# Kernel optimization log

Measured on AMD Instinct MI355X. Metric: run time of the kernel, lower is better.

## Reference

```python
import jax, jax.numpy as jnp
import numpy as np

B, C, H, W = 8, 256, 64, 64
RED = 16

def setup_inputs() -> dict:
    key = jax.random.key(0)
    ks = jax.random.split(key, 10)
    s = 0.05
    return {
        "x": jax.random.normal(ks[0], (B, C, H, W), jnp.float32),
        "ca_w1": jax.random.normal(ks[1], (C // RED, C), jnp.float32) * s,
        "ca_w2": jax.random.normal(ks[2], (C, C // RED), jnp.float32) * s,
        "q_w": jax.random.normal(ks[3], (C // RED, C), jnp.float32) * s,
        "q_b": jax.random.normal(ks[4], (C // RED,), jnp.float32) * s,
        "k_w": jax.random.normal(ks[5], (C // RED, C), jnp.float32) * s,
        "k_b": jax.random.normal(ks[6], (C // RED,), jnp.float32) * s,
        "v_w": jax.random.normal(ks[7], (C, C), jnp.float32) * s,
        "v_b": jax.random.normal(ks[8], (C,), jnp.float32) * s,
        "gamma": jax.random.normal(ks[9], (1,), jnp.float32) * s,
    }

def _cbam(x, ca_w1, ca_w2, q_w, q_b, k_w, k_b, v_w, v_b, gamma):
    # ---- Channel attention (squeeze-excite with avg+max pooling) ----
    avg = jnp.mean(x, axis=(2, 3))          # [B, C]
    mx = jnp.max(x, axis=(2, 3))            # [B, C]
    def fc(s):
        h = jax.nn.relu(jnp.einsum('rc,bc->br', ca_w1, s))
        return jnp.einsum('cr,br->bc', ca_w2, h)
    gate = jax.nn.sigmoid(fc(avg) + fc(mx))[:, :, None, None]
    x = x * gate
    # ---- Spatial (non-local) attention ----
    b, c, h, w = x.shape
    hw = h * w
    xf = x.reshape(b, c, hw)                          # [B, C, HW]
    q = jnp.einsum('rc,bcn->brn', q_w, xf) + q_b[None, :, None]   # [B, C/r, HW]
    k = jnp.einsum('rc,bcn->brn', k_w, xf) + k_b[None, :, None]
    v = jnp.einsum('oc,bcn->bon', v_w, xf) + v_b[None, :, None]   # [B, C, HW]
    attn = jax.nn.softmax(jnp.einsum('bri,brj->bij', q, k), axis=-1)  # [B, HW, HW]
    out = jnp.einsum('bcj,bij->bci', v, attn).reshape(b, c, h, w)
    return gamma[0] * out + x

def reference(x, ca_w1, ca_w2, q_w, q_b, k_w, k_b, v_w, v_b, gamma):
    return _cbam(x, ca_w1, ca_w2, q_w, q_b, k_w, k_b, v_w, v_b, gamma)
```

## Files before the change

kernel.cpp:

```cpp
#include <hip/hip_runtime.h>
#include <hip/hip_bf16.h>
#include <math.h>

#define BB 8
#define CCH 256
#define HWN 4096
#define RR 16

typedef __attribute__((ext_vector_type(8))) short short8;
typedef __attribute__((ext_vector_type(4))) float f32x4;

static __device__ __forceinline__ unsigned short f2bf(float x) {
    union { float f; unsigned u; } v; v.f = x;
    return (unsigned short)((v.u + 0x8000u) >> 16);
}

__global__ __launch_bounds__(256) void k_pool(const float* __restrict__ x,
                                              float* __restrict__ avgp,
                                              float* __restrict__ maxp,
                                              const float* __restrict__ vw,
                                              const float* __restrict__ qw,
                                              const float* __restrict__ kw,
                                              unsigned short* __restrict__ Wb) {
    int bc = blockIdx.x;
    int t = threadIdx.x;
    if (bc < 288) {
        int idx = bc * 256 + t;
        int m = idx >> 8, c = idx & 255;
        float v;
        if (m < 256) v = vw[idx];
        else if (m < 272) v = qw[(m - 256) * 256 + c];
        else v = kw[(m - 272) * 256 + c];
        Wb[idx] = f2bf(v);
    }
    const float4* p = (const float4*)(x + (size_t)bc * HWN);
    float s = 0.f, m = -INFINITY;
#pragma unroll
    for (int i = 0; i < 4; ++i) {
        float4 v = p[t + 256 * i];
        s += v.x + v.y + v.z + v.w;
        m = fmaxf(m, fmaxf(fmaxf(v.x, v.y), fmaxf(v.z, v.w)));
    }
    for (int off = 32; off; off >>= 1) {
        s += __shfl_down(s, off);
        m = fmaxf(m, __shfl_down(m, off));
    }
    __shared__ float ss[4], sm[4];
    int wid = t >> 6;
    if ((t & 63) == 0) { ss[wid] = s; sm[wid] = m; }
    __syncthreads();
    if (t == 0) {
        float S = ss[0] + ss[1] + ss[2] + ss[3];
        float M = fmaxf(fmaxf(sm[0], sm[1]), fmaxf(sm[2], sm[3]));
        avgp[bc] = S * (1.f / (float)HWN);
        maxp[bc] = M;
    }
}

__global__ __launch_bounds__(256) void k_gate(const float* __restrict__ avgp,
                                              const float* __restrict__ maxp,
                                              const float* __restrict__ w1,
                                              const float* __restrict__ w2,
                                              float* __restrict__ gate) {
    int b = blockIdx.x, t = threadIdx.x;
    __shared__ float sa[CCH], sx[CCH], sh[32];
    sa[t] = avgp[b * CCH + t];
    sx[t] = maxp[b * CCH + t];
    __syncthreads();
    if (t < 32) {
        int r = t & 15;
        const float* src = (t < 16) ? sa : sx;
        float h = 0.f;
        for (int c = 0; c < CCH; ++c) h += w1[r * CCH + c] * src[c];
        sh[t] = fmaxf(h, 0.f);
    }
    __syncthreads();
    float g = 0.f;
#pragma unroll
    for (int r = 0; r < RR; ++r) g += w2[t * RR + r] * (sh[r] + sh[16 + r]);
    gate[b * CCH + t] = 1.f / (1.f + __expf(-g));
}

__global__ __launch_bounds__(256) void k_proj(const float* __restrict__ x,
                                              const float* __restrict__ gate,
                                              const unsigned short* __restrict__ Wb,
                                              const float* __restrict__ vb,
                                              const float* __restrict__ qb,
                                              const float* __restrict__ kb,
                                              unsigned short* __restrict__ qT,
                                              unsigned short* __restrict__ kT,
                                              unsigned short* __restrict__ vB) {
    int b = blockIdx.x & 7;
    int n0 = (blockIdx.x >> 3) << 6;
    int t = threadIdx.x;
    int w = t >> 6, l = t & 63, quad = l >> 4, ln = l & 15;

    __shared__ __align__(16) unsigned short xs_t[64][72];
    __shared__ __align__(16) unsigned short vtile[256 * 72];
    __shared__ float qk_s[32][66];

    const f32x4 zf = {0.f, 0.f, 0.f, 0.f};
    f32x4 acc[18];
#pragma unroll
    for (int mt = 0; mt < 18; ++mt) acc[mt] = zf;

    for (int cc = 0; cc < 4; ++cc) {
        __syncthreads();
#pragma unroll
        for (int it = 0; it < 4; ++it) {
            int idx = it * 256 + t;
            int cl = idx >> 4, nq = idx & 15;
            int c = cc * 64 + cl;
            float g = gate[b * CCH + c];
            float4 v = *(const float4*)(x + (((size_t)(b * CCH + c)) << 12) + n0 + nq * 4);
            xs_t[nq * 4 + 0][cl] = f2bf(v.x * g);
            xs_t[nq * 4 + 1][cl] = f2bf(v.y * g);
            xs_t[nq * 4 + 2][cl] = f2bf(v.z * g);
            xs_t[nq * 4 + 3][cl] = f2bf(v.w * g);
        }
        __syncthreads();

        short8 bfrag[2];
#pragma unroll
        for (int kc = 0; kc < 2; ++kc)
            bfrag[kc] = *(const short8*)&xs_t[w * 16 + ln][kc * 32 + quad * 8];

#pragma unroll
        for (int mt = 0; mt < 18; ++mt) {
#pragma unroll
            for (int kc = 0; kc < 2; ++kc) {
                short8 af = *(const short8*)(Wb + ((size_t)(mt * 16 + ln)) * 256 + cc * 64 + kc * 32 + quad * 8);
                acc[mt] = __builtin_amdgcn_mfma_f32_16x16x32_bf16(af, bfrag[kc], acc[mt], 0, 0, 0);
            }
        }
    }

#pragma unroll
    for (int mt = 0; mt < 16; ++mt) {
#pragma unroll
        for (int r = 0; r < 4; ++r) {
            int m = mt * 16 + quad * 4 + r;
            vtile[m * 72 + w * 16 + ln] = f2bf(acc[mt][r] + vb[m]);
        }
    }
#pragma unroll
    for (int r = 0; r < 4; ++r) {
        qk_s[quad * 4 + r][w * 16 + ln] = acc[16][r];
        qk_s[16 + quad * 4 + r][w * 16 + ln] = acc[17][r];
    }
    __syncthreads();

    {
        unsigned short* vBp = vB + (((size_t)b) << 20);
        int c = t;
#pragma unroll
        for (int Q = 0; Q < 8; ++Q) {
            short8 v8 = *(const short8*)(vtile + c * 72 + Q * 8);
            *(short8*)(vBp + ((size_t)((((n0 >> 3) + Q) << 8) + c) << 3)) = v8;
        }
    }
    if (t < 128) {
        int isK = t >> 6;
        int n = t & 63;
        const float* bias = isK ? kb : qb;
        unsigned u32[8];
#pragma unroll
        for (int j = 0; j < 8; ++j) {
            unsigned lo = f2bf(qk_s[isK * 16 + 2 * j][n] + bias[2 * j]);
            unsigned hi = f2bf(qk_s[isK * 16 + 2 * j + 1][n] + bias[2 * j + 1]);
            u32[j] = lo | (hi << 16);
        }
        unsigned short* dst = (isK ? kT : qT) + ((size_t)(b * HWN + n0 + n)) * RR;
        uint4 d0 = {u32[0], u32[1], u32[2], u32[3]};
        uint4 d1 = {u32[4], u32[5], u32[6], u32[7]};
        ((uint4*)dst)[0] = d0;
        ((uint4*)dst)[1] = d1;
    }
}

__global__ __launch_bounds__(512, 4) void k_attn(const unsigned short* __restrict__ qT,
                                                 const unsigned short* __restrict__ kT,
                                                 const unsigned short* __restrict__ vB,
                                                 const float* __restrict__ x,
                                                 const float* __restrict__ gate,
                                                 const float* __restrict__ gamma,
                                                 float* __restrict__ out) {
    int b = blockIdx.x & 7;
    int i0 = (blockIdx.x >> 3) << 6;
    int t = threadIdx.x;
    int w = __builtin_amdgcn_readfirstlane(t >> 6);
    int l = t & 63;
    int quad = l >> 4, ln = l & 15;
    int jsub = w >> 1;
    int ih = w & 1;
    int c0 = w * 32;

    __shared__ __align__(16) unsigned short p_lds[4][4096];
    __shared__ float l_s[4][68];

    const short8 zs = {0, 0, 0, 0, 0, 0, 0, 0};
    const f32x4 zf = {0.f, 0.f, 0.f, 0.f};

    short8 bq[2];
    bq[0] = zs; bq[1] = zs;
    if (quad < 2) {
#pragma unroll
        for (int u = 0; u < 2; ++u)
            bq[u] = *(const short8*)(qT + (((size_t)(b * HWN + i0 + ih * 32 + u * 16 + ln)) << 4) + (quad << 3));
    }

    f32x4 acc[2][4];
#pragma unroll
    for (int cs = 0; cs < 2; ++cs)
#pragma unroll
        for (int is = 0; is < 4; ++is) acc[cs][is] = zf;
    float lsum[2] = {0.f, 0.f};

    const float c1 = 1.44269504f;
    const float c0e = -11.5415603f;

    const unsigned short* kb_u = kT + ((size_t)(b * HWN)) * RR;
    const int kln = ((jsub * 16 + ln) << 4) + (quad << 3);
    const unsigned short* vb_u = vB + (((size_t)b) << 20) + ((size_t)c0 << 3);
    int vln[4];
#pragma unroll
    for (int ks = 0; ks < 2; ++ks)
#pragma unroll
        for (int cs = 0; cs < 2; ++cs)
            vln[ks * 2 + cs] = (((ks * 4 + quad) << 8) + cs * 16 + ln) << 3;

    int soff = ((jsub * 2 + (quad >> 1)) * 64 + ih * 32 + ln) * 8 + (quad & 1) * 4;
    int rbase = quad * 512 + ln * 8;

    short8 akA = zs, akB = zs;
    short8 avA[4], avB[4];

    auto load_ak = [&](short8& ak, int j0) {
        if (quad < 2) ak = *(const short8*)(kb_u + ((j0 << 4) + kln));
    };
    auto load_av = [&](short8 (&av)[4], int j0) {
        const unsigned short* vp = vb_u + (j0 << 8);
#pragma unroll
        for (int u = 0; u < 4; ++u) av[u] = *(const short8*)(vp + vln[u]);
    };

    load_ak(akA, 0);
    load_ak(akB, 64);
    load_av(avA, 0);
    load_av(avB, 64);

    auto finish_s = [&](const f32x4& sf, unsigned short* pbuf, int u) {
        float p0 = exp2f(fmaf(sf[0], c1, c0e));
        float p1 = exp2f(fmaf(sf[1], c1, c0e));
        float p2 = exp2f(fmaf(sf[2], c1, c0e));
        float p3 = exp2f(fmaf(sf[3], c1, c0e));
        lsum[u] += (p0 + p1) + (p2 + p3);
        uint2 pk;
        asm("v_cvt_pk_bf16_f32 %0, %1, %2" : "=v"(pk.x) : "v"(p0), "v"(p1));
        asm("v_cvt_pk_bf16_f32 %0, %1, %2" : "=v"(pk.y) : "v"(p2), "v"(p3));
        *(uint2*)(pbuf + soff + u * 128) = pk;
    };

    auto pv = [&](const short8 (&av)[4], const unsigned short* pbuf) {
#pragma unroll
        for (int ks = 0; ks < 2; ++ks) {
            short8 bp[4];
#pragma unroll
            for (int is = 0; is < 4; ++is)
                bp[is] = *(const short8*)(pbuf + rbase + ks * 2048 + is * 128);
#pragma unroll
            for (int cs = 0; cs < 2; ++cs)
#pragma unroll
                for (int is = 0; is < 4; ++is)
                    acc[cs][is] = __builtin_amdgcn_mfma_f32_16x16x32_bf16(av[ks * 2 + cs], bp[is], acc[cs][is], 0, 0, 0);
        }
    };

    for (int jt = 0; jt < 32; ++jt) {
        unsigned short* pb0 = &p_lds[(jt & 1) * 2 + 0][0];
        unsigned short* pb1 = &p_lds[(jt & 1) * 2 + 1][0];

        f32x4 sf00 = __builtin_amdgcn_mfma_f32_16x16x32_bf16(akA, bq[0], zf, 0, 0, 0);
        f32x4 sf01 = __builtin_amdgcn_mfma_f32_16x16x32_bf16(akA, bq[1], zf, 0, 0, 0);
        f32x4 sf10 = __builtin_amdgcn_mfma_f32_16x16x32_bf16(akB, bq[0], zf, 0, 0, 0);
        f32x4 sf11 = __builtin_amdgcn_mfma_f32_16x16x32_bf16(akB, bq[1], zf, 0, 0, 0);
        finish_s(sf00, pb0, 0);
        finish_s(sf01, pb0, 1);
        finish_s(sf10, pb1, 0);
        finish_s(sf11, pb1, 1);

        __syncthreads();

        bool pf = jt < 31;
        int j0n = (jt + 1) << 7;
        if (pf) { load_ak(akA, j0n); load_ak(akB, j0n + 64); }

        pv(avA, pb0);
        if (pf) load_av(avA, j0n);
        pv(avB, pb1);
        if (pf) load_av(avB, j0n + 64);
    }

    lsum[0] += __shfl_xor(lsum[0], 16, 64);
    lsum[0] += __shfl_xor(lsum[0], 32, 64);
    lsum[1] += __shfl_xor(lsum[1], 16, 64);
    lsum[1] += __shfl_xor(lsum[1], 32, 64);
    if (l < 16) {
        l_s[jsub][ih * 32 + l] = lsum[0];
        l_s[jsub][ih * 32 + 16 + l] = lsum[1];
    }
    __syncthreads();

    float g = gamma[0];
    float rinv[4];
#pragma unroll
    for (int is = 0; is < 4; ++is) {
        int i = is * 16 + ln;
        float lf = (l_s[0][i] + l_s[1][i]) + (l_s[2][i] + l_s[3][i]);
        rinv[is] = g / lf;
    }

#pragma unroll
    for (int cs = 0; cs < 2; ++cs) {
#pragma unroll
        for (int r = 0; r < 4; ++r) {
            int c = c0 + cs * 16 + quad * 4 + r;
            float gc = gate[b * CCH + c];
            size_t rowoff = (((size_t)(b * CCH + c)) << 12) + i0;
            float* po = out + rowoff;
            const float* px = x + rowoff;
#pragma unroll
            for (int is = 0; is < 4; ++is) {
                int idx = is * 16 + ln;
                po[idx] = acc[cs][is][r] * rinv[is] + px[idx] * gc;
            }
        }
    }
}

extern "C" void kernel_launch(void* const* d_in, const int* in_sizes, int n_in,
                              void* d_out, int out_size, void* d_ws, size_t ws_size,
                              hipStream_t stream) {
    const float* x = (const float*)d_in[0];
    const float* w1 = (const float*)d_in[1];
    const float* w2 = (const float*)d_in[2];
    const float* qw = (const float*)d_in[3];
    const float* qb = (const float*)d_in[4];
    const float* kw = (const float*)d_in[5];
    const float* kb = (const float*)d_in[6];
    const float* vw = (const float*)d_in[7];
    const float* vb = (const float*)d_in[8];
    const float* gamma = (const float*)d_in[9];
    float* out = (float*)d_out;
    char* ws = (char*)d_ws;

    float* avgp = (float*)(ws);
    float* maxp = (float*)(ws + 8192);
    float* gate = (float*)(ws + 16384);
    unsigned short* Wb = (unsigned short*)(ws + 24576);
    unsigned short* qT = (unsigned short*)(ws + 24576 + 147456);
    unsigned short* kT = (unsigned short*)(ws + 24576 + 147456 + 1048576);
    unsigned short* vB = (unsigned short*)(ws + 24576 + 147456 + 2097152);

    k_pool<<<2048, 256, 0, stream>>>(x, avgp, maxp, vw, qw, kw, Wb);
    k_gate<<<8, 256, 0, stream>>>(avgp, maxp, w1, w2, gate);
    k_proj<<<512, 256, 0, stream>>>(x, gate, Wb, vb, qb, kb, qT, kT, vB);
    k_attn<<<512, 512, 0, stream>>>(qT, kT, vB, x, gate, gamma, out);
}
```

Baseline: 231.5 us.

## Double attention query tile to 128 rows and widen per-wave channel block

Each k_attn block now handles 128 query positions instead of 64. Each wave computes 64 channels by 64 query rows, where before it computed 32 channels. Every loaded K and V fragment therefore feeds twice as many MFMAs, which roughly halves global traffic for K and V per unit of output. In exchange, the block count drops from 512 to 256 and LDS for the P buffers doubles. Accumulator and V register use also doubles, so occupancy is reduced and register spilling becomes a risk.

```diff
diff --git a/kernel.cpp b/kernel.cpp
--- a/kernel.cpp
+++ b/kernel.cpp
@@ -178,7 +178,7 @@
     }
 }
 
-__global__ __launch_bounds__(512, 4) void k_attn(const unsigned short* __restrict__ qT,
+__global__ __launch_bounds__(512, 2) void k_attn(const unsigned short* __restrict__ qT,
                                                  const unsigned short* __restrict__ kT,
                                                  const unsigned short* __restrict__ vB,
                                                  const float* __restrict__ x,
@@ -186,62 +186,63 @@
                                                  const float* __restrict__ gamma,
                                                  float* __restrict__ out) {
     int b = blockIdx.x & 7;
-    int i0 = (blockIdx.x >> 3) << 6;
+    int i0 = (blockIdx.x >> 3) << 7;
     int t = threadIdx.x;
     int w = __builtin_amdgcn_readfirstlane(t >> 6);
     int l = t & 63;
     int quad = l >> 4, ln = l & 15;
-    int jsub = w >> 1;
+    int cg = w >> 1;
     int ih = w & 1;
-    int c0 = w * 32;
-
-    __shared__ __align__(16) unsigned short p_lds[4][4096];
-    __shared__ float l_s[4][68];
+    int c0 = cg * 64;
+
+    __shared__ __align__(16) unsigned short p_lds[4][8192];
+    __shared__ float l_s[4][132];
 
     const short8 zs = {0, 0, 0, 0, 0, 0, 0, 0};
     const f32x4 zf = {0.f, 0.f, 0.f, 0.f};
 
-    short8 bq[2];
-    bq[0] = zs; bq[1] = zs;
+    short8 bq[4];
+#pragma unroll
+    for (int u = 0; u < 4; ++u) bq[u] = zs;
     if (quad < 2) {
 #pragma unroll
-        for (int u = 0; u < 2; ++u)
-            bq[u] = *(const short8*)(qT + (((size_t)(b * HWN + i0 + ih * 32 + u * 16 + ln)) << 4) + (quad << 3));
-    }
-
-    f32x4 acc[2][4];
-#pragma unroll
-    for (int cs = 0; cs < 2; ++cs)
+        for (int u = 0; u < 4; ++u)
+            bq[u] = *(const short8*)(qT + (((size_t)(b * HWN + i0 + ih * 64 + u * 16 + ln)) << 4) + (quad << 3));
+    }
+
+    f32x4 acc[4][4];
+#pragma unroll
+    for (int cs = 0; cs < 4; ++cs)
 #pragma unroll
         for (int is = 0; is < 4; ++is) acc[cs][is] = zf;
-    float lsum[2] = {0.f, 0.f};
+    float lsum[4] = {0.f, 0.f, 0.f, 0.f};
 
     const float c1 = 1.44269504f;
     const float c0e = -11.5415603f;
 
     const unsigned short* kb_u = kT + ((size_t)(b * HWN)) * RR;
-    const int kln = ((jsub * 16 + ln) << 4) + (quad << 3);
+    const int kln = ((cg * 16 + ln) << 4) + (quad << 3);
     const unsigned short* vb_u = vB + (((size_t)b) << 20) + ((size_t)c0 << 3);
-    int vln[4];
+    int vln[8];
 #pragma unroll
     for (int ks = 0; ks < 2; ++ks)
 #pragma unroll
-        for (int cs = 0; cs < 2; ++cs)
-            vln[ks * 2 + cs] = (((ks * 4 + quad) << 8) + cs * 16 + ln) << 3;
-
-    int soff = ((jsub * 2 + (quad >> 1)) * 64 + ih * 32 + ln) * 8 + (quad & 1) * 4;
-    int rbase = quad * 512 + ln * 8;
+        for (int cs = 0; cs < 4; ++cs)
+            vln[ks * 4 + cs] = (((ks * 4 + quad) << 8) + cs * 16 + ln) << 3;
+
+    int soff = ((cg * 2 + (quad >> 1)) * 128 + ih * 64 + ln) * 8 + (quad & 1) * 4;
+    int rbase = (quad * 128 + ih * 64 + ln) * 8;
 
     short8 akA = zs, akB = zs;
-    short8 avA[4], avB[4];
+    short8 avA[8], avB[8];
 
     auto load_ak = [&](short8& ak, int j0) {
         if (quad < 2) ak = *(const short8*)(kb_u + ((j0 << 4) + kln));
     };
-    auto load_av = [&](short8 (&av)[4], int j0) {
+    auto load_av = [&](short8 (&av)[8], int j0) {
         const unsigned short* vp = vb_u + (j0 << 8);
 #pragma unroll
-        for (int u = 0; u < 4; ++u) av[u] = *(const short8*)(vp + vln[u]);
+        for (int u = 0; u < 8; ++u) av[u] = *(const short8*)(vp + vln[u]);
     };
 
     load_ak(akA, 0);
@@ -261,18 +262,18 @@
         *(uint2*)(pbuf + soff + u * 128) = pk;
     };
 
-    auto pv = [&](const short8 (&av)[4], const unsigned short* pbuf) {
+    auto pv = [&](const short8 (&av)[8], const unsigned short* pbuf) {
 #pragma unroll
         for (int ks = 0; ks < 2; ++ks) {
             short8 bp[4];
 #pragma unroll
             for (int is = 0; is < 4; ++is)
-                bp[is] = *(const short8*)(pbuf + rbase + ks * 2048 + is * 128);
-#pragma unroll
-            for (int cs = 0; cs < 2; ++cs)
+                bp[is] = *(const short8*)(pbuf + rbase + ks * 4096 + is * 128);
+#pragma unroll
+            for (int cs = 0; cs < 4; ++cs)
 #pragma unroll
                 for (int is = 0; is < 4; ++is)
-                    acc[cs][is] = __builtin_amdgcn_mfma_f32_16x16x32_bf16(av[ks * 2 + cs], bp[is], acc[cs][is], 0, 0, 0);
+                    acc[cs][is] = __builtin_amdgcn_mfma_f32_16x16x32_bf16(av[ks * 4 + cs], bp[is], acc[cs][is], 0, 0, 0);
         }
     };
 
@@ -280,14 +281,17 @@
         unsigned short* pb0 = &p_lds[(jt & 1) * 2 + 0][0];
         unsigned short* pb1 = &p_lds[(jt & 1) * 2 + 1][0];
 
-        f32x4 sf00 = __builtin_amdgcn_mfma_f32_16x16x32_bf16(akA, bq[0], zf, 0, 0, 0);
-        f32x4 sf01 = __builtin_amdgcn_mfma_f32_16x16x32_bf16(akA, bq[1], zf, 0, 0, 0);
-        f32x4 sf10 = __builtin_amdgcn_mfma_f32_16x16x32_bf16(akB, bq[0], zf, 0, 0, 0);
-        f32x4 sf11 = __builtin_amdgcn_mfma_f32_16x16x32_bf16(akB, bq[1], zf, 0, 0, 0);
-        finish_s(sf00, pb0, 0);
-        finish_s(sf01, pb0, 1);
-        finish_s(sf10, pb1, 0);
-        finish_s(sf11, pb1, 1);
+        f32x4 sA[4], sB[4];
+#pragma unroll
+        for (int u = 0; u < 4; ++u)
+            sA[u] = __builtin_amdgcn_mfma_f32_16x16x32_bf16(akA, bq[u], zf, 0, 0, 0);
+#pragma unroll
+        for (int u = 0; u < 4; ++u)
+            sB[u] = __builtin_amdgcn_mfma_f32_16x16x32_bf16(akB, bq[u], zf, 0, 0, 0);
+#pragma unroll
+        for (int u = 0; u < 4; ++u) finish_s(sA[u], pb0, u);
+#pragma unroll
+        for (int u = 0; u < 4; ++u) finish_s(sB[u], pb1, u);
 
         __syncthreads();
 
@@ -301,13 +305,15 @@
         if (pf) load_av(avB, j0n + 64);
     }
 
-    lsum[0] += __shfl_xor(lsum[0], 16, 64);
-    lsum[0] += __shfl_xor(lsum[0], 32, 64);
-    lsum[1] += __shfl_xor(lsum[1], 16, 64);
-    lsum[1] += __shfl_xor(lsum[1], 32, 64);
+    #pragma unroll
+    for (int u = 0; u < 4; ++u) {
+        lsum[u] += __shfl_xor(lsum[u], 16, 64);
+        lsum[u] += __shfl_xor(lsum[u], 32, 64);
+    }
     if (l < 16) {
-        l_s[jsub][ih * 32 + l] = lsum[0];
-        l_s[jsub][ih * 32 + 16 + l] = lsum[1];
+#pragma unroll
+        for (int u = 0; u < 4; ++u)
+            l_s[cg][ih * 64 + u * 16 + l] = lsum[u];
     }
     __syncthreads();
 
@@ -315,13 +321,13 @@
     float rinv[4];
 #pragma unroll
     for (int is = 0; is < 4; ++is) {
-        int i = is * 16 + ln;
+        int i = ih * 64 + is * 16 + ln;
         float lf = (l_s[0][i] + l_s[1][i]) + (l_s[2][i] + l_s[3][i]);
         rinv[is] = g / lf;
     }
 
 #pragma unroll
-    for (int cs = 0; cs < 2; ++cs) {
+    for (int cs = 0; cs < 4; ++cs) {
 #pragma unroll
         for (int r = 0; r < 4; ++r) {
             int c = c0 + cs * 16 + quad * 4 + r;
@@ -331,7 +337,7 @@
             const float* px = x + rowoff;
 #pragma unroll
             for (int is = 0; is < 4; ++is) {
-                int idx = is * 16 + ln;
+                int idx = ih * 64 + is * 16 + ln;
                 po[idx] = acc[cs][is][r] * rinv[is] + px[idx] * gc;
             }
         }
@@ -365,5 +371,5 @@
     k_pool<<<2048, 256, 0, stream>>>(x, avgp, maxp, vw, qw, kw, Wb);
     k_gate<<<8, 256, 0, stream>>>(avgp, maxp, w1, w2, gate);
     k_proj<<<512, 256, 0, stream>>>(x, gate, Wb, vb, qb, kb, qT, kT, vB);
-    k_attn<<<512, 512, 0, stream>>>(qT, kT, vB, x, gate, gamma, out);
-}
+    k_attn<<<256, 512, 0, stream>>>(qT, kT, vB, x, gate, gamma, out);
+}
```

Result: no change. 233.6 us (+0.9%).

## Prefetch next x chunk into registers and halve v staging LDS in k_proj

Applied to the files above, without the earlier changes.

The projection kernel now loads the next channel chunk of x into registers while the MFMA loop for the current chunk runs, hiding global load latency behind compute. The V output staging tile is cut from 256 to 128 channel rows and written out in two halves with extra barriers, and launch bounds request 4 blocks per CU. Together these shrink LDS use so more blocks can be resident. The cost is extra registers for the prefetch buffers, which may conflict with the occupancy target, plus additional syncthreads.

```diff
diff --git a/kernel.cpp b/kernel.cpp
--- a/kernel.cpp
+++ b/kernel.cpp
@@ -81,28 +81,39 @@
     gate[b * CCH + t] = 1.f / (1.f + __expf(-g));
 }
 
-__global__ __launch_bounds__(256) void k_proj(const float* __restrict__ x,
-                                              const float* __restrict__ gate,
-                                              const unsigned short* __restrict__ Wb,
-                                              const float* __restrict__ vb,
-                                              const float* __restrict__ qb,
-                                              const float* __restrict__ kb,
-                                              unsigned short* __restrict__ qT,
-                                              unsigned short* __restrict__ kT,
-                                              unsigned short* __restrict__ vB) {
+__global__ __launch_bounds__(256, 4) void k_proj(const float* __restrict__ x,
+                                                 const float* __restrict__ gate,
+                                                 const unsigned short* __restrict__ Wb,
+                                                 const float* __restrict__ vb,
+                                                 const float* __restrict__ qb,
+                                                 const float* __restrict__ kb,
+                                                 unsigned short* __restrict__ qT,
+                                                 unsigned short* __restrict__ kT,
+                                                 unsigned short* __restrict__ vB) {
     int b = blockIdx.x & 7;
     int n0 = (blockIdx.x >> 3) << 6;
     int t = threadIdx.x;
     int w = t >> 6, l = t & 63, quad = l >> 4, ln = l & 15;
 
     __shared__ __align__(16) unsigned short xs_t[64][72];
-    __shared__ __align__(16) unsigned short vtile[256 * 72];
+    __shared__ __align__(16) unsigned short vtile[128 * 72];
     __shared__ float qk_s[32][66];
 
     const f32x4 zf = {0.f, 0.f, 0.f, 0.f};
     f32x4 acc[18];
 #pragma unroll
     for (int mt = 0; mt < 18; ++mt) acc[mt] = zf;
+
+    const float* xp[4];
+#pragma unroll
+    for (int it = 0; it < 4; ++it) {
+        int idx = it * 256 + t;
+        int cl = idx >> 4, nq = idx & 15;
+        xp[it] = x + (((size_t)(b * CCH + cl)) << 12) + n0 + nq * 4;
+    }
+    float4 xr[4];
+#pragma unroll
+    for (int it = 0; it < 4; ++it) xr[it] = *(const float4*)xp[it];
 
     for (int cc = 0; cc < 4; ++cc) {
         __syncthreads();
@@ -112,7 +123,7 @@
             int cl = idx >> 4, nq = idx & 15;
             int c = cc * 64 + cl;
             float g = gate[b * CCH + c];
-            float4 v = *(const float4*)(x + (((size_t)(b * CCH + c)) << 12) + n0 + nq * 4);
+            float4 v = xr[it];
             xs_t[nq * 4 + 0][cl] = f2bf(v.x * g);
             xs_t[nq * 4 + 1][cl] = f2bf(v.y * g);
             xs_t[nq * 4 + 2][cl] = f2bf(v.z * g);
@@ -120,6 +131,12 @@
         }
         __syncthreads();
 
+        if (cc < 3) {
+#pragma unroll
+            for (int it = 0; it < 4; ++it)
+                xr[it] = *(const float4*)(xp[it] + (((size_t)(cc + 1)) << 18));
+        }
+
         short8 bfrag[2];
 #pragma unroll
         for (int kc = 0; kc < 2; ++kc)
@@ -135,8 +152,11 @@
         }
     }
 
-#pragma unroll
-    for (int mt = 0; mt < 16; ++mt) {
+    unsigned short* vBp = vB + (((size_t)b) << 20);
+    int ch = t & 127, Qh = (t >> 7) * 4;
+
+#pragma unroll
+    for (int mt = 0; mt < 8; ++mt) {
 #pragma unroll
         for (int r = 0; r < 4; ++r) {
             int m = mt * 16 + quad * 4 + r;
@@ -149,16 +169,30 @@
         qk_s[16 + quad * 4 + r][w * 16 + ln] = acc[17][r];
     }
     __syncthreads();
-
-    {
-        unsigned short* vBp = vB + (((size_t)b) << 20);
-        int c = t;
-#pragma unroll
-        for (int Q = 0; Q < 8; ++Q) {
-            short8 v8 = *(const short8*)(vtile + c * 72 + Q * 8);
-            *(short8*)(vBp + ((size_t)((((n0 >> 3) + Q) << 8) + c) << 3)) = v8;
-        }
-    }
+#pragma unroll
+    for (int qq = 0; qq < 4; ++qq) {
+        int Q = Qh + qq;
+        short8 v8 = *(const short8*)(vtile + ch * 72 + Q * 8);
+        *(short8*)(vBp + ((size_t)((((n0 >> 3) + Q) << 8) + ch) << 3)) = v8;
+    }
+    __syncthreads();
+
+#pragma unroll
+    for (int mt = 8; mt < 16; ++mt) {
+#pragma unroll
+        for (int r = 0; r < 4; ++r) {
+            int m = mt * 16 + quad * 4 + r;
+            vtile[(m - 128) * 72 + w * 16 + ln] = f2bf(acc[mt][r] + vb[m]);
+        }
+    }
+    __syncthreads();
+#pragma unroll
+    for (int qq = 0; qq < 4; ++qq) {
+        int Q = Qh + qq;
+        short8 v8 = *(const short8*)(vtile + ch * 72 + Q * 8);
+        *(short8*)(vBp + ((size_t)((((n0 >> 3) + Q) << 8) + (128 + ch)) << 3)) = v8;
+    }
+
     if (t < 128) {
         int isK = t >> 6;
         int n = t & 63;
```

After: 241.7 us. +4.4%, slower.
